# Optimization experiments

Hardware: AMD Instinct MI355X
Metric: run time of the kernel (lower is better)

Reference implementation:

```python
import jax, jax.numpy as jnp
import numpy as np

DIM_IN = 1024
DIM_QK = 1024
DIM_V = 1024


def setup_inputs() -> dict:
    key = jax.random.key(0)
    ks = jax.random.split(key, 8)
    s = DIM_IN ** -0.5
    return {
        "x": jax.random.normal(ks[0], (16, 2048, DIM_IN), dtype=jnp.float32),
        "encoder_output": jax.random.normal(ks[1], (16, 2048, DIM_IN), dtype=jnp.float32),
        "W_q": jax.random.normal(ks[2], (DIM_IN, DIM_QK), dtype=jnp.float32) * s,
        "b_q": jnp.zeros((DIM_QK,), dtype=jnp.float32),
        "W_k": jax.random.normal(ks[3], (DIM_IN, DIM_QK), dtype=jnp.float32) * s,
        "b_k": jnp.zeros((DIM_QK,), dtype=jnp.float32),
        "W_v": jax.random.normal(ks[4], (DIM_IN, DIM_V), dtype=jnp.float32) * s,
        "b_v": jnp.zeros((DIM_V,), dtype=jnp.float32),
    }


def reference(x, encoder_output, W_q, b_q, W_k, b_k, W_v, b_v):
    # Q: [B, Lq, Dqk]; K, V: [B, Lk, Dqk/Dv]
    Q = x @ W_q + b_q
    K = encoder_output @ W_k + b_k
    V = encoder_output @ W_v + b_v
    # attn_scores: [B, Lq, Lk], scaled by 1/sqrt(Dqk)
    scores = jnp.einsum("bqd,bkd->bqk", Q, K) * (K.shape[-1] ** -0.5)
    weights = jax.nn.softmax(scores, axis=-1)
    H = jnp.einsum("bqk,bkv->bqv", weights, V)  # [B, Lq, Dv]
    return H
```

## Files before the change

kernel.cpp:

```cpp
#include <hip/hip_runtime.h>

typedef _Float16 f16;
typedef __attribute__((ext_vector_type(4))) _Float16 f16x4;
typedef __attribute__((ext_vector_type(8))) _Float16 f16x8;
typedef __attribute__((ext_vector_type(4))) float f32x4;

#define MFMA16(a, b, c) __builtin_amdgcn_mfma_f32_16x16x32_f16(a, b, c, 0, 0, 0)

__device__ __forceinline__ void gll16(const void* g, void* l) {
    __builtin_amdgcn_global_load_lds(
        (const __attribute__((address_space(1))) unsigned int*)g,
        (__attribute__((address_space(3))) unsigned int*)l, 16, 0, 0);
}

#define BAR() __builtin_amdgcn_s_barrier()
#define LGKM(n) do { asm volatile("s_waitcnt lgkmcnt(" #n ")" ::: "memory"); \
                     __builtin_amdgcn_sched_barrier(0); } while (0)
#define VMC(n)  do { asm volatile("s_waitcnt vmcnt(" #n ")" ::: "memory"); \
                     __builtin_amdgcn_sched_barrier(0); } while (0)

__global__ __launch_bounds__(256) void cvt_f16(
    const float* __restrict__ in, f16* __restrict__ out)
{
    const size_t i = ((size_t)blockIdx.x * 256 + threadIdx.x) * 8;
    float4 a = *(const float4*)(in + i);
    float4 b = *(const float4*)(in + i + 4);
    f16x8 o;
    o[0] = (f16)a.x; o[1] = (f16)a.y; o[2] = (f16)a.z; o[3] = (f16)a.w;
    o[4] = (f16)b.x; o[5] = (f16)b.y; o[6] = (f16)b.z; o[7] = (f16)b.w;
    *(f16x8*)(out + i) = o;
}

__global__ __launch_bounds__(256) void prep_weights(
    const float* __restrict__ Wq, const float* __restrict__ Wk,
    const float* __restrict__ Wv, f16* __restrict__ Wt)
{
    __shared__ float tile[32][33];
    const float* W = blockIdx.z == 0 ? Wq : (blockIdx.z == 1 ? Wk : Wv);
    f16* dst = Wt + (size_t)blockIdx.z * 1024 * 1024;
    const int tx = threadIdx.x & 31, ty = threadIdx.x >> 5;
    const int n0 = blockIdx.x * 32, k0 = blockIdx.y * 32;
#pragma unroll
    for (int i = 0; i < 4; i++)
        tile[ty + i * 8][tx] = W[(size_t)(k0 + ty + i * 8) * 1024 + n0 + tx];
    __syncthreads();
#pragma unroll
    for (int i = 0; i < 4; i++)
        dst[(size_t)(n0 + ty + i * 8) * 1024 + k0 + tx] = (f16)tile[tx][ty + i * 8];
}

template <int KD, int EPI>
__global__ __launch_bounds__(512, 2) void gemm8(
    const f16* __restrict__ Ab, const f16* __restrict__ Bb,
    const float* __restrict__ b0, const float* __restrict__ b1, float scale,
    void* __restrict__ C0, void* __restrict__ C1, float* __restrict__ aux,
    size_t strA, size_t strB, size_t strC, int ldc, int nbx, int nby)
{
    __shared__ f16 shA[2][256 * 64];
    __shared__ f16 shB[2][256 * 64];

    int id = blockIdx.x;
    {
        const int chunk = (int)gridDim.x >> 3;
        id = (id & 7) * chunk + (id >> 3);
    }
    const int by = id % nby;
    const int r2 = id / nby;
    const int bx = r2 % nbx;
    const int z  = r2 / nbx;
    const int bm = bx * 256, bn = by * 256;

    const f16* A = Ab + (size_t)z * strA;
    const f16* B = Bb + (size_t)z * strB;

    const int t = threadIdx.x, lane = t & 63, wid = t >> 6;
    const int wr = wid >> 2, wc = wid & 3;
    const int fr = lane & 15, kb = (lane >> 4) * 16;
    const int sw = (fr & 7) << 4;

    const int lsr = lane >> 3;
    const int lsc = ((lane & 7) * 16) ^ (lsr << 4);
    const int a_  = wid * 8;
    const int bq_ = (wid >> 2) * 64 + (wid & 3) * 8;
    const f16* aT = A + (size_t)(bm + lsr) * KD + (lsc >> 1);
    const f16* bT = B + (size_t)(bn + lsr) * KD + (lsc >> 1);

#define STG_A0(d, kt) do {                                                    \
        const f16* As_ = aT + (size_t)(kt) * 64; f16* da_ = &shA[d][0];       \
        gll16(As_ + (size_t)(a_)*KD,        da_ + (a_)*64);                   \
        gll16(As_ + (size_t)(128 + a_)*KD,  da_ + (128 + a_)*64); } while (0)
#define STG_A1(d, kt) do {                                                    \
        const f16* As_ = aT + (size_t)(kt) * 64; f16* da_ = &shA[d][0];       \
        gll16(As_ + (size_t)(64 + a_)*KD,   da_ + (64 + a_)*64);              \
        gll16(As_ + (size_t)(192 + a_)*KD,  da_ + (192 + a_)*64); } while (0)
#define STG_B0(d, kt) do {                                                    \
        const f16* Bs_ = bT + (size_t)(kt) * 64; f16* db_ = &shB[d][0];       \
        gll16(Bs_ + (size_t)(bq_)*KD,       db_ + (bq_)*64);                  \
        gll16(Bs_ + (size_t)(128 + bq_)*KD, db_ + (128 + bq_)*64); } while (0)
#define STG_B1(d, kt) do {                                                    \
        const f16* Bs_ = bT + (size_t)(kt) * 64; f16* db_ = &shB[d][0];       \
        gll16(Bs_ + (size_t)(32 + bq_)*KD,  db_ + (32 + bq_)*64);             \
        gll16(Bs_ + (size_t)(160 + bq_)*KD, db_ + (160 + bq_)*64); } while (0)

    f16x8 af[2][2][4];
    f16x8 bf[2][2][2];
    f32x4 acc[8][4] = {};

#define LDA(mh)                                                               \
    _Pragma("unroll") for (int kk_ = 0; kk_ < 2; ++kk_)                       \
    _Pragma("unroll") for (int i_ = 0; i_ < 4; ++i_)                          \
        af[mh][kk_][i_] = *(const f16x8*)(sAc +                               \
            (wr * 128 + (mh) * 64 + i_ * 16 + fr) * 128 +                     \
            (((kk_ << 6) | kb) ^ sw));

#define LDB(nh)                                                               \
    _Pragma("unroll") for (int kk_ = 0; kk_ < 2; ++kk_)                       \
    _Pragma("unroll") for (int j_ = 0; j_ < 2; ++j_)                          \
        bf[nh][kk_][j_] = *(const f16x8*)(sBc +                               \
            (wc * 64 + (nh) * 32 + j_ * 16 + fr) * 128 +                      \
            (((kk_ << 6) | kb) ^ sw));

#define MM(mh, nh)                                                            \
    __builtin_amdgcn_s_setprio(1);                                            \
    _Pragma("unroll") for (int kk_ = 0; kk_ < 2; ++kk_)                       \
    _Pragma("unroll") for (int i_ = 0; i_ < 4; ++i_)                          \
    _Pragma("unroll") for (int j_ = 0; j_ < 2; ++j_)                          \
        acc[(mh) * 4 + i_][(nh) * 2 + j_] =                                   \
            MFMA16(af[mh][kk_][i_], bf[nh][kk_][j_],                          \
                   acc[(mh) * 4 + i_][(nh) * 2 + j_]);                        \
    __builtin_amdgcn_s_setprio(0);

    constexpr int NT = KD / 64;

    STG_A0(0, 0); STG_B0(0, 0); STG_B1(0, 0); STG_A1(0, 0);
    VMC(4);
    BAR();

    for (int ti = 0; ti < NT; ++ti) {
        const int c = ti & 1;
        const int n = c ^ 1;
        const int kn = ti + 1;
        const bool pf = (kn < NT);
        const char* sAc = (const char*)&shA[c][0];
        const char* sBc = (const char*)&shB[c][0];
        LDA(0); LDB(0);
        if (pf) { STG_A0(n, kn); VMC(4); } else { VMC(2); }
        BAR(); LGKM(0); MM(0, 0); BAR();
        LDB(1);
        if (pf) { STG_B0(n, kn); VMC(4); } else { VMC(0); }
        BAR(); LGKM(0); MM(0, 1); BAR();
        LDA(1);
        if (pf) STG_B1(n, kn);
        BAR(); LGKM(0); MM(1, 1); BAR();
        if (pf) { STG_A1(n, kn); VMC(4); }
        BAR(); MM(1, 0); BAR();
    }

    const int fc = lane & 15, rq = (lane >> 4) * 4;

    if constexpr (EPI == 2) {
        BAR();
        float* part = (float*)&shA[0][0];
        f16* Sp = (f16*)C0 + (size_t)z * strC;
#pragma unroll
        for (int mi = 0; mi < 8; ++mi)
#pragma unroll
            for (int r = 0; r < 4; ++r) {
                const int rl = wr * 128 + mi * 16 + rq + r;
                float ps = 0.f;
#pragma unroll
                for (int nj = 0; nj < 4; ++nj) {
                    const int col = bn + wc * 64 + nj * 16 + fc;
                    f16 eh = (f16)__expf(acc[mi][nj][r]);
                    ps += (float)eh;
                    Sp[(size_t)(bm + rl) * ldc + col] = eh;
                }
#pragma unroll
                for (int o = 1; o < 16; o <<= 1) ps += __shfl_xor(ps, o);
                if (fc == 0) part[rl * 4 + wc] = ps;
            }
        BAR();
        if (t < 256) {
            const float4 p4 = *(const float4*)(part + t * 4);
            aux[((size_t)z * 2048 + bm + t) * 8 + by] = p4.x + p4.y + p4.z + p4.w;
        }
        return;
    }

#pragma unroll
    for (int nj = 0; nj < 4; ++nj) {
        const int col = bn + wc * 64 + nj * 16 + fc;
        float bv_ = 0.f;
        if constexpr (EPI == 0) bv_ = b0[col];
        if constexpr (EPI == 1) bv_ = (col < 1024) ? b0[col] : b1[col - 1024];
#pragma unroll
        for (int mi = 0; mi < 8; ++mi) {
            if constexpr (EPI == 1) {
                if (col >= 1024) {
                    const int rowb = bm + wr * 128 + mi * 16 + rq;
                    f16x4 q;
#pragma unroll
                    for (int r = 0; r < 4; ++r) q[r] = (f16)(acc[mi][nj][r] + bv_);
                    f16* Cp = (f16*)C1 + (size_t)(rowb >> 11) * 2048 * 1024 +
                              (size_t)(col - 1024) * 2048;
                    *(f16x4*)&Cp[rowb & 2047] = q;
                    continue;
                }
            }
#pragma unroll
            for (int r = 0; r < 4; ++r) {
                const int row = bm + wr * 128 + mi * 16 + rq + r;
                float v = acc[mi][nj][r];
                if constexpr (EPI == 0) v = (v + bv_) * scale;
                if constexpr (EPI == 1) v = v + bv_;
                if constexpr (EPI == 3) v *= aux[(size_t)z * 2048 + row];
                if constexpr (EPI == 0) {
                    ((f16*)C0)[(size_t)row * ldc + col] = (f16)v;
                } else if constexpr (EPI == 1) {
                    ((f16*)C0)[(size_t)row * 1024 + col] = (f16)v;
                } else {
                    ((float*)C0 + (size_t)z * strC)[(size_t)row * ldc + col] = v;
                }
            }
        }
    }
#undef STG_A0
#undef STG_A1
#undef STG_B0
#undef STG_B1
#undef LDA
#undef LDB
#undef MM
}

__global__ __launch_bounds__(256) void rowinv_k(
    const float* __restrict__ part, float* __restrict__ inv)
{
    const int q = blockIdx.x * 256 + threadIdx.x;
    const float4* p = (const float4*)(part + (size_t)q * 8);
    const float4 a = p[0], b = p[1];
    inv[q] = 1.0f / (a.x + a.y + a.z + a.w + b.x + b.y + b.z + b.w);
}

extern "C" void kernel_launch(void* const* d_in, const int* in_sizes, int n_in,
                              void* d_out, int out_size, void* d_ws, size_t ws_size,
                              hipStream_t stream)
{
    const float* x   = (const float*)d_in[0];
    const float* enc = (const float*)d_in[1];
    const float* Wq  = (const float*)d_in[2];
    const float* bq  = (const float*)d_in[3];
    const float* Wk  = (const float*)d_in[4];
    const float* bk  = (const float*)d_in[5];
    const float* Wv  = (const float*)d_in[6];
    const float* bv  = (const float*)d_in[7];

    const size_t TOK = (size_t)16 * 2048;
    f16* Qh = (f16*)d_ws;
    f16* Kh = Qh + TOK * 1024;
    f16* Vt = Kh + TOK * 1024;
    f16* Wt = Vt + TOK * 1024;
    f16* S  = Wt + (size_t)3 * 1024 * 1024;
    f16* Xh = S;
    f16* Eh = S + TOK * 1024;
    float* Ppart = (float*)Wt;
    float* Rinv  = Ppart + TOK * 8;

    cvt_f16<<<16384, 256, 0, stream>>>(x,   Xh);
    cvt_f16<<<16384, 256, 0, stream>>>(enc, Eh);

    prep_weights<<<dim3(32, 32, 3), 256, 0, stream>>>(Wq, Wk, Wv, Wt);

    gemm8<1024, 0><<<512, 512, 0, stream>>>(
        Xh, Wt, bq, nullptr, 0.03125f, Qh, nullptr, nullptr,
        0, 0, 0, 1024, 128, 4);

    gemm8<1024, 1><<<1024, 512, 0, stream>>>(
        Eh, Wt + (size_t)1024 * 1024, bk, bv, 1.0f, Kh, Vt, nullptr,
        0, 0, 0, 1024, 128, 8);

    gemm8<1024, 2><<<1024, 512, 0, stream>>>(
        Qh, Kh, nullptr, nullptr, 1.0f, S, nullptr, Ppart,
        (size_t)2048 * 1024, (size_t)2048 * 1024, (size_t)2048 * 2048, 2048, 8, 8);

    rowinv_k<<<128, 256, 0, stream>>>(Ppart, Rinv);

    gemm8<2048, 3><<<512, 512, 0, stream>>>(
        S, Vt, nullptr, nullptr, 1.0f, d_out, nullptr, Rinv,
        (size_t)2048 * 2048, (size_t)1024 * 2048, (size_t)2048 * 1024, 1024, 8, 4);
}
```

Before: 657.5 us.

## Restructure GEMM k-loop to a single barrier per tile with interleaved prefetch

Replaces the four-phase main loop, which had eight barriers and explicit lgkmcnt waits per k-tile, with a schedule that reads LDS fragments per k-half and issues the next tile's global-to-LDS loads between MFMA groups. There is now one vmcnt(0) wait and one barrier at the end of each tile. Explicit waits and scheduling barriers are removed and the compiler orders LDS reads. The aim is to cut barrier and wait overhead and let MFMAs overlap with loads. In exchange, the full vmcnt drain at the end of each tile may expose global load latency, and more fragment registers are live at once.

New measurement: 696.8 us. 6.0% more time.

```diff
diff --git a/kernel.cpp b/kernel.cpp
--- a/kernel.cpp
+++ b/kernel.cpp
@@ -14,10 +14,7 @@
 }
 
 #define BAR() __builtin_amdgcn_s_barrier()
-#define LGKM(n) do { asm volatile("s_waitcnt lgkmcnt(" #n ")" ::: "memory"); \
-                     __builtin_amdgcn_sched_barrier(0); } while (0)
-#define VMC(n)  do { asm volatile("s_waitcnt vmcnt(" #n ")" ::: "memory"); \
-                     __builtin_amdgcn_sched_barrier(0); } while (0)
+#define VMC(n)  asm volatile("s_waitcnt vmcnt(" #n ")" ::: "memory")
 
 __global__ __launch_bounds__(256) void cvt_f16(
     const float* __restrict__ in, f16* __restrict__ out)
@@ -106,54 +103,52 @@
     f16x8 bf[2][2][2];
     f32x4 acc[8][4] = {};
 
-#define LDA(mh)                                                               \
-    _Pragma("unroll") for (int kk_ = 0; kk_ < 2; ++kk_)                       \
+#define RD_A(mh, kk)                                                          \
     _Pragma("unroll") for (int i_ = 0; i_ < 4; ++i_)                          \
-        af[mh][kk_][i_] = *(const f16x8*)(sAc +                               \
+        af[mh][kk][i_] = *(const f16x8*)(sAc +                                \
             (wr * 128 + (mh) * 64 + i_ * 16 + fr) * 128 +                     \
-            (((kk_ << 6) | kb) ^ sw));
-
-#define LDB(nh)                                                               \
-    _Pragma("unroll") for (int kk_ = 0; kk_ < 2; ++kk_)                       \
+            ((((kk) << 6) | kb) ^ sw));
+
+#define RD_B(nh, kk)                                                          \
     _Pragma("unroll") for (int j_ = 0; j_ < 2; ++j_)                          \
-        bf[nh][kk_][j_] = *(const f16x8*)(sBc +                               \
+        bf[nh][kk][j_] = *(const f16x8*)(sBc +                                \
             (wc * 64 + (nh) * 32 + j_ * 16 + fr) * 128 +                      \
-            (((kk_ << 6) | kb) ^ sw));
-
-#define MM(mh, nh)                                                            \
+            ((((kk) << 6) | kb) ^ sw));
+
+#define MM8(mh, nh, kk)                                                       \
     __builtin_amdgcn_s_setprio(1);                                            \
-    _Pragma("unroll") for (int kk_ = 0; kk_ < 2; ++kk_)                       \
     _Pragma("unroll") for (int i_ = 0; i_ < 4; ++i_)                          \
     _Pragma("unroll") for (int j_ = 0; j_ < 2; ++j_)                          \
         acc[(mh) * 4 + i_][(nh) * 2 + j_] =                                   \
-            MFMA16(af[mh][kk_][i_], bf[nh][kk_][j_],                          \
+            MFMA16(af[mh][kk][i_], bf[nh][kk][j_],                            \
                    acc[(mh) * 4 + i_][(nh) * 2 + j_]);                        \
     __builtin_amdgcn_s_setprio(0);
 
     constexpr int NT = KD / 64;
 
     STG_A0(0, 0); STG_B0(0, 0); STG_B1(0, 0); STG_A1(0, 0);
-    VMC(4);
+    VMC(0);
     BAR();
 
     for (int ti = 0; ti < NT; ++ti) {
         const int c = ti & 1;
-        const int n = c ^ 1;
+        const bool pf = (ti + 1 < NT);
         const int kn = ti + 1;
-        const bool pf = (kn < NT);
         const char* sAc = (const char*)&shA[c][0];
         const char* sBc = (const char*)&shB[c][0];
-        LDA(0); LDB(0);
-        if (pf) { STG_A0(n, kn); VMC(4); } else { VMC(2); }
-        BAR(); LGKM(0); MM(0, 0); BAR();
-        LDB(1);
-        if (pf) { STG_B0(n, kn); VMC(4); } else { VMC(0); }
-        BAR(); LGKM(0); MM(0, 1); BAR();
-        LDA(1);
-        if (pf) STG_B1(n, kn);
-        BAR(); LGKM(0); MM(1, 1); BAR();
-        if (pf) { STG_A1(n, kn); VMC(4); }
-        BAR(); MM(1, 0); BAR();
+        RD_B(0, 0); RD_A(0, 0); RD_B(1, 0); RD_A(1, 0);
+        MM8(0, 0, 0);
+        if (pf) STG_A0(c ^ 1, kn);
+        MM8(0, 1, 0);
+        if (pf) STG_B0(c ^ 1, kn);
+        RD_B(0, 1); RD_A(0, 1); RD_B(1, 1); RD_A(1, 1);
+        MM8(1, 1, 0);
+        if (pf) STG_B1(c ^ 1, kn);
+        MM8(1, 0, 0);
+        if (pf) STG_A1(c ^ 1, kn);
+        MM8(0, 0, 1); MM8(0, 1, 1); MM8(1, 1, 1); MM8(1, 0, 1);
+        VMC(0);
+        BAR();
     }
 
     const int fc = lane & 15, rq = (lane >> 4) * 4;
@@ -228,9 +223,9 @@
 #undef STG_A1
 #undef STG_B0
 #undef STG_B1
-#undef LDA
-#undef LDB
-#undef MM
+#undef RD_A
+#undef RD_B
+#undef MM8
 }
 
 __global__ __launch_bounds__(256) void rowinv_k(
```
